# Performance work log

Hardware: AMD Instinct MI355X
Metric: run time of the kernel (lower is better)

Reference implementation:

```python
import jax, jax.numpy as jnp
import numpy as np

NEG = -1e4      # BigBird additive mask value
LN_EPS = 1e-12  # BERT-style LayerNorm eps


def _bigbird_forward(xs_pad, mask, Wq, bq, Wk, bk, Wv, bv, Wo, bo, gamma, beta, rand_idx):
    b, n, hsz = xs_pad.shape
    H = rand_idx.shape[0]
    nb = rand_idx.shape[1] + 2          # one rand row per non-edge query block
    BS = n // nb                        # block size
    d = hsz // H
    r = rand_idx.shape[2]
    scale = 1.0 / np.sqrt(d).astype(np.float32)

    mf = mask.reshape(b, n).astype(xs_pad.dtype)   # (b,n) 1=token, 0=pad
    mb = mf.reshape(b, nb, BS)                     # blocked mask

    def proj(W, bias):
        return (xs_pad @ W + bias).reshape(b, n, H, d).transpose(0, 2, 1, 3)

    q = proj(Wq, bq) * scale            # (b,H,n,d)
    k = proj(Wk, bk)
    v = proj(Wv, bv)
    qb = q.reshape(b, H, nb, BS, d)
    kb = k.reshape(b, H, nb, BS, d)
    vb = v.reshape(b, H, nb, BS, d)

    # ---- global rows: first / last query block attend to all keys ----
    def full_row(qi):                   # qi: (b,H,BS,d)
        s = jnp.einsum('bhqd,bhkd->bhqk', qi, k) + (1.0 - mf)[:, None, None, :] * NEG
        return jnp.einsum('bhqk,bhkd->bhqd', jax.nn.softmax(s, axis=-1), v)

    ctx_first = full_row(qb[:, :, 0])
    ctx_last = full_row(qb[:, :, nb - 1])

    # ---- random key/value blocks: per-head, per-query-block gather ----
    hidx = jnp.arange(H)[:, None, None]
    rand_k = kb[:, hidx, rand_idx].reshape(b, H, nb - 2, r * BS, d)
    rand_v = vb[:, hidx, rand_idx].reshape(b, H, nb - 2, r * BS, d)
    rand_m = mb[:, rand_idx].reshape(b, H, nb - 2, r * BS)

    def sparse_row(qi, kc, vc, mc):     # kc:(b,H,K,d), mc:(b,H,K)
        s = jnp.einsum('bhqd,bhkd->bhqk', qi, kc) + (1.0 - mc)[:, :, None, :] * NEG
        return jnp.einsum('bhqk,bhkd->bhqd', jax.nn.softmax(s, axis=-1), vc)

    def gather_blocks(ids, ridx):
        kc = jnp.concatenate([kb[:, :, j] for j in ids] + [rand_k[:, :, ridx]], axis=2)
        vc = jnp.concatenate([vb[:, :, j] for j in ids] + [rand_v[:, :, ridx]], axis=2)
        mc = jnp.concatenate([jnp.broadcast_to(mb[:, None, j], (b, H, BS)) for j in ids]
                             + [rand_m[:, :, ridx]], axis=2)
        return kc, vc, mc

    # second / penultimate query blocks: window + globals + rand
    ctx_second = sparse_row(qb[:, :, 1], *gather_blocks([0, 1, 2, nb - 1], 0))
    ctx_penult = sparse_row(qb[:, :, nb - 2], *gather_blocks([nb - 3, nb - 2, nb - 1, 0], nb - 3))

    # ---- middle rows i in [2, nb-3]: 3-block sliding window + first/last global + r random ----
    nmid = nb - 4
    mid = jnp.arange(2, nb - 2)
    win = mid[:, None] + jnp.arange(-1, 2)[None, :]        # (nmid,3)
    k_win = kb[:, :, win].reshape(b, H, nmid, 3 * BS, d)
    v_win = vb[:, :, win].reshape(b, H, nmid, 3 * BS, d)
    m_win = jnp.broadcast_to(mb[:, win].reshape(b, 1, nmid, 3 * BS), (b, H, nmid, 3 * BS))

    def rep_glob(t):                     # (b,H,BS,...) -> (b,H,nmid,BS,...)
        return jnp.broadcast_to(t[:, :, None], (b, H, nmid) + t.shape[2:])

    k_mid = jnp.concatenate([k_win, rep_glob(kb[:, :, 0]), rep_glob(kb[:, :, nb - 1]),
                             rand_k[:, :, 1:nb - 3]], axis=3)
    v_mid = jnp.concatenate([v_win, rep_glob(vb[:, :, 0]), rep_glob(vb[:, :, nb - 1]),
                             rand_v[:, :, 1:nb - 3]], axis=3)
    m_first = jnp.broadcast_to(mb[:, None, None, 0], (b, H, nmid, BS))
    m_last = jnp.broadcast_to(mb[:, None, None, nb - 1], (b, H, nmid, BS))
    m_mid = jnp.concatenate([m_win, m_first, m_last, rand_m[:, :, 1:nb - 3]], axis=3)

    s_mid = jnp.einsum('bhmqd,bhmkd->bhmqk', qb[:, :, 2:nb - 2], k_mid) \
            + (1.0 - m_mid)[:, :, :, None, :] * NEG
    ctx_mid = jnp.einsum('bhmqk,bhmkd->bhmqd', jax.nn.softmax(s_mid, axis=-1), v_mid)

    ctx = jnp.concatenate([ctx_first[:, :, None], ctx_second[:, :, None], ctx_mid,
                           ctx_penult[:, :, None], ctx_last[:, :, None]], axis=2)
    ctx = ctx.reshape(b, H, n, d).transpose(0, 2, 1, 3).reshape(b, n, hsz)
    ctx = ctx * mf[:, :, None]           # from_mask on output rows

    # BigBirdSelfOutput: dense + residual + LayerNorm (dropout=0 / eval)
    y = ctx @ Wo + bo + xs_pad
    mu = y.mean(-1, keepdims=True)
    var = ((y - mu) ** 2).mean(-1, keepdims=True)
    return (y - mu) * jax.lax.rsqrt(var + LN_EPS) * gamma + beta


def setup_inputs() -> dict:
    key = jax.random.key(0)
    ks = jax.random.split(key, 6)
    B, N, HSZ, H, BS, R = 4, 4096, 1024, 16, 64, 3
    NB = N // BS
    init = lambda k, shp: jax.random.normal(k, shp, dtype=jnp.float32) * 0.02
    return {
        'xs_pad': jax.random.normal(ks[0], (B, N, HSZ), dtype=jnp.float32),
        'mask': jnp.ones((B, 1, N), dtype=jnp.int32),
        'Wq': init(ks[1], (HSZ, HSZ)), 'bq': jnp.zeros((HSZ,), jnp.float32),
        'Wk': init(ks[2], (HSZ, HSZ)), 'bk': jnp.zeros((HSZ,), jnp.float32),
        'Wv': init(ks[3], (HSZ, HSZ)), 'bv': jnp.zeros((HSZ,), jnp.float32),
        'Wo': init(ks[4], (HSZ, HSZ)), 'bo': jnp.zeros((HSZ,), jnp.float32),
        'gamma': jnp.ones((HSZ,), jnp.float32), 'beta': jnp.zeros((HSZ,), jnp.float32),
        'rand_idx': jax.random.randint(ks[5], (H, NB - 2, R), 1, NB - 1).astype(jnp.int32),
    }


def reference(xs_pad, mask, Wq, bq, Wk, bk, Wv, bv, Wo, bo, gamma, beta, rand_idx):
    return _bigbird_forward(xs_pad, mask, Wq, bq, Wk, bk, Wv, bv, Wo, bo, gamma, beta, rand_idx)
```

## Files before the change

### kernel.cpp

```cpp
#include <hip/hip_runtime.h>
#include <hip/hip_bf16.h>

#define B_   4
#define N_   4096
#define HSZ  1024
#define H_   16
#define D_   64
#define NB_  64
#define R_   3
#define M_   (B_*N_)
#define NEGV (-1e4f)
#define LOG2E 1.4426950408889634f

typedef float f32x4 __attribute__((ext_vector_type(4)));
typedef short s16x8 __attribute__((ext_vector_type(8)));
typedef __bf16 b16x8 __attribute__((ext_vector_type(8)));

__device__ __forceinline__ f32x4 mfma16(s16x8 a, s16x8 b, f32x4 c) {
  return __builtin_amdgcn_mfma_f32_16x16x32_bf16(
      __builtin_bit_cast(b16x8, a), __builtin_bit_cast(b16x8, b), c, 0, 0, 0);
}

__device__ __forceinline__ short f2b(float x) {
  __hip_bfloat16 h = __float2bfloat16(x);
  return (short)__builtin_bit_cast(unsigned short, h);
}

__device__ __forceinline__ unsigned pack2(float a, float b) {
  return (unsigned)(unsigned short)f2b(a) |
         ((unsigned)(unsigned short)f2b(b) << 16);
}

__device__ __forceinline__ void gl_lds16(const short* g, short* l) {
  __builtin_amdgcn_global_load_lds(
      (const __attribute__((address_space(1))) unsigned int*)g,
      (__attribute__((address_space(3))) unsigned int*)l, 16, 0, 0);
}

__global__ __launch_bounds__(256) void k_prep(const float* __restrict__ in,
                                              short* __restrict__ out,
                                              const float* __restrict__ Wq,
                                              const float* __restrict__ Wk,
                                              const float* __restrict__ Wv,
                                              const float* __restrict__ Wo,
                                              short* __restrict__ wt) {
  const int tid = threadIdx.x;
  if (blockIdx.x < 8192) {
    size_t i = ((size_t)blockIdx.x * 256 + tid) * 8;
    float4 a = *(const float4*)&in[i];
    float4 b = *(const float4*)&in[i + 4];
    s16x8 o;
    o[0] = f2b(a.x); o[1] = f2b(a.y); o[2] = f2b(a.z); o[3] = f2b(a.w);
    o[4] = f2b(b.x); o[5] = f2b(b.y); o[6] = f2b(b.z); o[7] = f2b(b.w);
    *(s16x8*)&out[i] = o;
    return;
  }
  const int bid = blockIdx.x - 8192;
  const int z = bid >> 8;
  const int rest = bid & 255;
  const int tk = (rest >> 4) * 64, tn = (rest & 15) * 64;
  const float* src = (z == 0) ? Wq : (z == 1) ? Wk : (z == 2) ? Wv : Wo;
  short* dst = wt + (size_t)z * HSZ * HSZ;
  __shared__ __align__(16) float t[64][68];
#pragma unroll
  for (int r = 0; r < 4; ++r) {
    int c = tid + r * 256;
    int row = c >> 4, seg = c & 15;
    *(float4*)&t[row][seg * 4] =
        *(const float4*)&src[(size_t)(tk + row) * HSZ + tn + seg * 4];
  }
  __syncthreads();
#pragma unroll
  for (int r = 0; r < 2; ++r) {
    int c = tid + r * 256;
    int row = c >> 3, seg = c & 7;
    s16x8 o;
#pragma unroll
    for (int u = 0; u < 8; ++u) o[u] = f2b(t[seg * 8 + u][row]);
    *(s16x8*)&dst[(size_t)(tn + row) * HSZ + tk + seg * 8] = o;
  }
}

template <bool SWAP>
__device__ __forceinline__ void gemm8_core(
    const short* __restrict__ A, const short* __restrict__ Bt, int tm, int tn,
    short (&a_lds)[2][256][64], short (&b_lds)[2][256][64],
    f32x4 (&acc)[8][4], int wave, int lane) {
  const int lq = lane & 15, g = lane >> 4;
  const int wm = wave >> 2, wn = wave & 3;
  const int sl8 = lane >> 3;
  const int sc = ((lane & 7) ^ sl8) * 8;

  auto ST_A = [&](int buf, int kt) {
#pragma unroll
    for (int h = 0; h < 2; ++h)
#pragma unroll
      for (int u = 0; u < 2; ++u) {
        const int rbase = h * 128 + wave * 8 + u * 64;
        gl_lds16(&A[(size_t)(tm + rbase + sl8) * HSZ + kt * 64 + sc],
                 &a_lds[buf][rbase][0]);
      }
  };
  auto ST_B = [&](int buf, int kt) {
#pragma unroll
    for (int h = 0; h < 2; ++h)
#pragma unroll
      for (int u = 0; u < 2; ++u) {
        const int rbase = h * 128 + wave * 8 + u * 64;
        gl_lds16(&Bt[(size_t)(tn + rbase + sl8) * HSZ + kt * 64 + sc],
                 &b_lds[buf][rbase][0]);
      }
  };

  s16x8 bf[4][2];
  auto LOADB = [&](int buf) {
#pragma unroll
    for (int j = 0; j < 4; ++j) {
      const int row = wn * 64 + j * 16 + lq;
#pragma unroll
      for (int kk = 0; kk < 2; ++kk)
        bf[j][kk] =
            *(const s16x8*)&b_lds[buf][row][((kk * 4 + g) ^ (lq & 7)) * 8];
    }
  };
  s16x8 afc[2][2], afn[2][2];
  auto LOADA = [&](int buf, int m0, s16x8 (&af)[2][2]) {
#pragma unroll
    for (int i = 0; i < 2; ++i) {
      const int row = wm * 128 + (m0 + i) * 16 + lq;
#pragma unroll
      for (int kk = 0; kk < 2; ++kk)
        af[i][kk] =
            *(const s16x8*)&a_lds[buf][row][((kk * 4 + g) ^ (lq & 7)) * 8];
    }
  };
  auto MF = [&](s16x8 (&af)[2][2], int m0) {
    __builtin_amdgcn_s_setprio(1);
#pragma unroll
    for (int i = 0; i < 2; ++i)
#pragma unroll
      for (int j = 0; j < 4; ++j)
#pragma unroll
        for (int kk = 0; kk < 2; ++kk)
          acc[m0 + i][j] = SWAP
                               ? mfma16(bf[j][kk], af[i][kk], acc[m0 + i][j])
                               : mfma16(af[i][kk], bf[j][kk], acc[m0 + i][j]);
    __builtin_amdgcn_s_setprio(0);
    __builtin_amdgcn_s_barrier();
  };

  ST_A(0, 0);
  ST_B(0, 0);
  ST_B(1, 1);

  for (int p = 0; p < 8; ++p) {
    const int t = 2 * p;
    ST_A(1, t + 1);
    asm volatile("s_waitcnt vmcnt(8)" ::: "memory");
    __builtin_amdgcn_s_barrier();
    LOADB(0);
    LOADA(0, 0, afc);
    LOADA(0, 2, afn);
    MF(afc, 0);
    if (t + 2 < 16) ST_B(0, t + 2);
    LOADA(0, 4, afc);
    MF(afn, 2);
    LOADA(0, 6, afn);
    MF(afc, 4);
    MF(afn, 6);
    if (t + 2 < 16) ST_A(0, t + 2);
    if (p < 7) {
      asm volatile("s_waitcnt vmcnt(8)" ::: "memory");
    } else {
      asm volatile("s_waitcnt vmcnt(0)" ::: "memory");
    }
    __builtin_amdgcn_s_barrier();
    LOADB(1);
    LOADA(1, 0, afc);
    LOADA(1, 2, afn);
    MF(afc, 0);
    if (t + 3 < 16) ST_B(1, t + 3);
    LOADA(1, 4, afc);
    MF(afn, 2);
    LOADA(1, 6, afn);
    MF(afc, 4);
    MF(afn, 6);
  }
}

__global__ __launch_bounds__(512) void k_qkv(
    const short* __restrict__ A, const short* __restrict__ WT,
    const float* __restrict__ bq, const float* __restrict__ bk,
    const float* __restrict__ bv, short* __restrict__ oq,
    short* __restrict__ ok, short* __restrict__ ovt) {
  const int orig = blockIdx.x;
  const int xcd = orig & 7, r = orig >> 3;
  const int combo = r >> 3, tml = r & 7;
  const int z = combo >> 2, tnl = combo & 3;
  const int tm = (xcd * 8 + tml) * 256, tn = tnl * 256;
  const short* Bt = WT + (size_t)z * HSZ * HSZ;

  __shared__ __align__(16) short a_lds[2][256][64];
  __shared__ __align__(16) short b_lds[2][256][64];

  const int tid = threadIdx.x, lane = tid & 63, wave = tid >> 6;
  const int lq = lane & 15, g = lane >> 4;
  const int wm = wave >> 2, wn = wave & 3;

  f32x4 acc[8][4] = {};

  if (z == 2) {
    gemm8_core<false>(A, Bt, tm, tn, a_lds, b_lds, acc, wave, lane);
#pragma unroll
    for (int j = 0; j < 4; ++j) {
      const int col = tn + wn * 64 + j * 16 + lq;
      const int hh = col >> 6, dd = col & 63;
      const float bi = bv[col];
#pragma unroll
      for (int i = 0; i < 8; ++i) {
        const int nrow = tm + wm * 128 + i * 16 + g * 4;
        const int bb = nrow >> 12, nn = nrow & (N_ - 1);
        uint2 w;
        w.x = pack2(acc[i][j][0] + bi, acc[i][j][1] + bi);
        w.y = pack2(acc[i][j][2] + bi, acc[i][j][3] + bi);
        *(uint2*)&ovt[(((size_t)bb * H_ + hh) * D_ + dd) * N_ + nn] = w;
      }
    }
  } else {
    gemm8_core<true>(A, Bt, tm, tn, a_lds, b_lds, acc, wave, lane);
    const float* bias = z ? bk : bq;
    short* outb = z ? ok : oq;
    const float alpha = z ? 1.0f : 0.125f * LOG2E;
#pragma unroll
    for (int i = 0; i < 8; ++i) {
      const int row = tm + wm * 128 + i * 16 + lq;
#pragma unroll
      for (int j = 0; j < 4; ++j) {
        const int colb = tn + wn * 64 + j * 16 + g * 4;
        const float4 bi = *(const float4*)&bias[colb];
        const int bb = row >> 12, nn = row & (N_ - 1);
        const int hh = colb >> 6, dd = colb & 63;
        uint2 w;
        w.x = pack2((acc[i][j][0] + bi.x) * alpha,
                    (acc[i][j][1] + bi.y) * alpha);
        w.y = pack2((acc[i][j][2] + bi.z) * alpha,
                    (acc[i][j][3] + bi.w) * alpha);
        *(uint2*)&outb[(((size_t)bb * H_ + hh) * N_ + nn) * D_ + dd] = w;
      }
    }
  }
}

__global__ __launch_bounds__(512) void k_out(
    const short* __restrict__ A, const short* __restrict__ WT,
    const float* __restrict__ bo, const float* __restrict__ xs,
    float* __restrict__ yout) {
  const short* Bt = WT + (size_t)3 * HSZ * HSZ;

  __shared__ __align__(16) short a_lds[2][256][64];
  __shared__ __align__(16) short b_lds[2][256][64];

  const int tid = threadIdx.x, lane = tid & 63, wave = tid >> 6;
  const int lq = lane & 15, g = lane >> 4;
  const int wm = wave >> 2, wn = wave & 3;
  const int orig = blockIdx.x;
  const int xcd = orig & 7, r = orig >> 3;
  const int tnl = r >> 3, tml = r & 7;
  const int tm = (xcd * 8 + tml) * 256, tn = tnl * 256;

  f32x4 acc[8][4] = {};
  gemm8_core<true>(A, Bt, tm, tn, a_lds, b_lds, acc, wave, lane);

#pragma unroll
  for (int i = 0; i < 8; ++i) {
    const int row = tm + wm * 128 + i * 16 + lq;
#pragma unroll
    for (int j = 0; j < 4; ++j) {
      const int colb = tn + wn * 64 + j * 16 + g * 4;
      const float4 bi = *(const float4*)&bo[colb];
      const size_t idx = (size_t)row * HSZ + colb;
      const float4 xv = *(const float4*)&xs[idx];
      float4 yv;
      yv.x = acc[i][j][0] + bi.x + xv.x;
      yv.y = acc[i][j][1] + bi.y + xv.y;
      yv.z = acc[i][j][2] + bi.z + xv.z;
      yv.w = acc[i][j][3] + bi.w + xv.w;
      *(float4*)&yout[idx] = yv;
    }
  }
}

__global__ __launch_bounds__(256) void k_attn(
    const short* __restrict__ Q, const short* __restrict__ K,
    const short* __restrict__ VT, const int* __restrict__ mask,
    const int* __restrict__ rnd, short* __restrict__ ctx,
    float* __restrict__ pO, float* __restrict__ pm, float* __restrict__ pl) {
  const int orig = blockIdx.x;
  const int swg = (orig & 7) * 624 + (orig >> 3);
  const int s = swg % 78;
  const int bh_i = swg / 78;
  const int h = bh_i & 15, b = bh_i >> 4;
  const int tid = threadIdx.x, lane = tid & 63, wave = tid >> 6;
  const int g = lane >> 4, lq = lane & 15;

  __shared__ __align__(16) short k_lds[2][64][64];
  __shared__ __align__(16) short vt_lds[2][64][64];
  __shared__ __align__(16) short p_lds[4][16][72];
  __shared__ __align__(16) float bias_s[8][64];
  __shared__ int list_s[8];
  __shared__ int Ls;

  const bool mid = (s < 62);
  const int qb = mid ? (s + 1) : (((s - 62) >> 3) ? (NB_ - 1) : 0);

  if (tid == 0) {
    int L;
    if (!mid) {
      int chunk = (s - 62) & 7;
#pragma unroll
      for (int i = 0; i < 8; ++i) list_s[i] = chunk * 8 + i;
      L = 8;
    } else {
      const int* rp = rnd + ((size_t)h * (NB_ - 2) + (qb - 1)) * R_;
      int n;
      if (qb == 1) {
        list_s[0] = 0; list_s[1] = 1; list_s[2] = 2; list_s[3] = NB_ - 1; n = 4;
      } else if (qb == NB_ - 2) {
        list_s[0] = NB_ - 3; list_s[1] = NB_ - 2; list_s[2] = NB_ - 1;
        list_s[3] = 0; n = 4;
      } else {
        list_s[0] = qb - 1; list_s[1] = qb; list_s[2] = qb + 1;
        list_s[3] = 0; list_s[4] = NB_ - 1; n = 5;
      }
      for (int j = 0; j < R_; ++j) list_s[n + j] = rp[j];
      L = n + R_;
      for (int i = L; i < 8; ++i) list_s[i] = 0;
    }
    Ls = L;
  }

  const size_t bh = (size_t)b * H_ + h;
  const size_t qrow = bh * N_ + (size_t)qb * 64 + wave * 16 + lq;
  s16x8 qf0 = *(const s16x8*)&Q[qrow * D_ + g * 8];
  s16x8 qf1 = *(const s16x8*)&Q[qrow * D_ + 32 + g * 8];

  __syncthreads();
  const int L = Ls;

  const int sw = (lq & 7);
  const int sl8 = lane >> 3;
  const int scg = ((lane & 7) ^ sl8) * 8;

  const short* Kb = K + bh * (size_t)N_ * D_;
  const short* Vb = VT + bh * (size_t)D_ * N_;
  const int* mb = mask + (size_t)b * N_;

  for (int t = tid; t < 512; t += 256) {
    const int i = t >> 6, kk2 = t & 63;
    bias_s[i][kk2] =
        (1.0f - (float)mb[list_s[i] * 64 + kk2]) * (NEGV * LOG2E);
  }
  asm volatile("s_waitcnt lgkmcnt(0)" ::: "memory");

  auto STAGE = [&](int buf, int kb) {
    const short* kp = Kb + (size_t)kb * 64 * D_;
    const short* vp = Vb + (size_t)kb * 64;
#pragma unroll
    for (int u = 0; u < 2; ++u) {
      const int rb = wave * 16 + u * 8;
      gl_lds16(&kp[(size_t)(rb + sl8) * D_ + scg], &k_lds[buf][rb][0]);
      gl_lds16(&vp[(size_t)(rb + sl8) * N_ + scg], &vt_lds[buf][rb][0]);
    }
  };

  s16x8 ones;
#pragma unroll
  for (int u = 0; u < 8; ++u) ones[u] = (short)0x3F80;

  f32x4 o[4] = {};
  f32x4 osum = {};
  float mshift = 0.0f;

  STAGE(0, list_s[0]);

  for (int it = 0; it < L; ++it) {
    const int buf = it & 1;
    if (it + 1 < L) {
      STAGE(buf ^ 1, list_s[it + 1]);
      asm volatile("s_waitcnt vmcnt(4)" ::: "memory");
    } else {
      asm volatile("s_waitcnt vmcnt(0)" ::: "memory");
    }
    __builtin_amdgcn_s_barrier();

    f32x4 st[4];
#pragma unroll
    for (int f = 0; f < 4; ++f) {
      f32x4 a0 = *(const f32x4*)&bias_s[it][f * 16 + g * 4];
      s16x8 af0 = *(const s16x8*)&k_lds[buf][f * 16 + lq][(g ^ sw) * 8];
      s16x8 af1 = *(const s16x8*)&k_lds[buf][f * 16 + lq][((4 + g) ^ sw) * 8];
      a0 = mfma16(af0, qf0, a0);
      a0 = mfma16(af1, qf1, a0);
      st[f] = a0;
    }

    if (mshift == 0.0f) {
#pragma unroll
      for (int f = 0; f < 4; ++f)
#pragma unroll
        for (int e = 0; e < 4; ++e) st[f][e] = exp2f(st[f][e]);
    } else {
#pragma unroll
      for (int f = 0; f < 4; ++f)
#pragma unroll
        for (int e = 0; e < 4; ++e) st[f][e] = exp2f(st[f][e] - mshift);
    }

#pragma unroll
    for (int f = 0; f < 4; ++f) {
      uint2 w = make_uint2(pack2(st[f][0], st[f][1]),
                           pack2(st[f][2], st[f][3]));
      *(uint2*)&p_lds[wave][lq][f * 16 + g * 4] = w;
    }

#pragma unroll
    for (int kk = 0; kk < 2; ++kk) {
      s16x8 pa = *(const s16x8*)&p_lds[wave][lq][kk * 32 + g * 8];
#pragma unroll
      for (int j = 0; j < 4; ++j) {
        s16x8 bv =
            *(const s16x8*)&vt_lds[buf][j * 16 + lq][((kk * 4 + g) ^ sw) * 8];
        o[j] = mfma16(pa, bv, o[j]);
      }
      osum = mfma16(pa, ones, osum);
    }

    float om = fmaxf(fmaxf(osum[0], osum[1]), fmaxf(osum[2], osum[3]));
    if (__any(om > 16777216.0f)) {
#pragma unroll
      for (int j = 0; j < 4; ++j) o[j] *= 5.9604645e-08f;
      osum *= 5.9604645e-08f;
      mshift += 24.0f;
    }
    __builtin_amdgcn_s_barrier();
  }

  if (mid) {
    float rs[4];
#pragma unroll
    for (int e = 0; e < 4; ++e)
      rs[e] = (float)mb[qb * 64 + wave * 16 + g * 4 + e] /
              fmaxf(osum[e], 1e-30f);
    __syncthreads();
    short (*ost)[64] = k_lds[0];
#pragma unroll
    for (int j = 0; j < 4; ++j) {
      ost[wave * 16 + g * 4 + 0][j * 16 + lq] = f2b(o[j][0] * rs[0]);
      ost[wave * 16 + g * 4 + 1][j * 16 + lq] = f2b(o[j][1] * rs[1]);
      ost[wave * 16 + g * 4 + 2][j * 16 + lq] = f2b(o[j][2] * rs[2]);
      ost[wave * 16 + g * 4 + 3][j * 16 + lq] = f2b(o[j][3] * rs[3]);
    }
    __syncthreads();
#pragma unroll
    for (int pp = 0; pp < 2; ++pp) {
      int c = tid + pp * 256;
      int row = c >> 3, seg = c & 7;
      *(s16x8*)&ctx[((size_t)b * N_ + qb * 64 + row) * HSZ + h * D_ + seg * 8] =
          *(const s16x8*)&ost[row][seg * 8];
    }
  } else {
    const int e2 = s - 62;
    const int qsel = e2 >> 3, chunk = e2 & 7;
    const size_t eidx = (bh * 2 + qsel) * 8 + chunk;
    float* po = pO + eidx * 4096;
#pragma unroll
    for (int j = 0; j < 4; ++j)
#pragma unroll
      for (int e = 0; e < 4; ++e)
        po[(wave * 16 + g * 4 + e) * 64 + j * 16 + lq] = o[j][e];
    if (lq == 0) {
#pragma unroll
      for (int e = 0; e < 4; ++e) {
        pm[eidx * 64 + wave * 16 + g * 4 + e] = mshift;
        pl[eidx * 64 + wave * 16 + g * 4 + e] = osum[e];
      }
    }
  }
}

__global__ __launch_bounds__(256) void k_comb(
    const float* __restrict__ pO, const float* __restrict__ pm,
    const float* __restrict__ pl, const int* __restrict__ mask,
    short* __restrict__ ctx) {
  const int qsel = blockIdx.x, h = blockIdx.y, b = blockIdx.z;
  const int qb = qsel ? NB_ - 1 : 0;
  const int tid = threadIdx.x;
  const int q = tid >> 2, dq = tid & 3;
  const size_t base = (((size_t)b * H_ + h) * 2 + qsel) * 8;

  float mv[8];
  float M = -INFINITY;
#pragma unroll
  for (int i = 0; i < 8; ++i) {
    mv[i] = pm[(base + i) * 64 + q];
    M = fmaxf(M, mv[i]);
  }
  float Lsum = 0.0f;
#pragma unroll
  for (int i = 0; i < 8; ++i) {
    float w = exp2f(mv[i] - M);
    mv[i] = w;
    Lsum += pl[(base + i) * 64 + q] * w;
  }
  f32x4 acc[4] = {};
#pragma unroll
  for (int i = 0; i < 8; ++i) {
    const float* p = pO + (base + i) * 4096 + q * 64 + dq * 16;
    float w = mv[i];
#pragma unroll
    for (int u = 0; u < 4; ++u) {
      f32x4 v = *(const f32x4*)&p[u * 4];
      acc[u] += v * w;
    }
  }
  float sc = (float)mask[(size_t)b * N_ + qb * 64 + q] / fmaxf(Lsum, 1e-30f);
  s16x8 out0, out1;
#pragma unroll
  for (int u = 0; u < 8; ++u) {
    out0[u] = f2b(acc[u >> 2][u & 3] * sc);
    out1[u] = f2b(acc[2 + (u >> 2)][u & 3] * sc);
  }
  short* dst = &ctx[((size_t)b * N_ + qb * 64 + q) * HSZ + h * D_ + dq * 16];
  *(s16x8*)dst = out0;
  *(s16x8*)(dst + 8) = out1;
}

__global__ __launch_bounds__(256) void k_ln(float* __restrict__ y,
                                            const float* __restrict__ gamma,
                                            const float* __restrict__ beta) {
  const int row = blockIdx.x, tid = threadIdx.x, lane = tid & 63,
            wave = tid >> 6;
  __shared__ float s_sum[4], s_sq[4];
  float4 v = *(const float4*)&y[(size_t)row * HSZ + tid * 4];
  float s = v.x + v.y + v.z + v.w;
  float q = v.x * v.x + v.y * v.y + v.z * v.z + v.w * v.w;
#pragma unroll
  for (int m = 1; m <= 32; m <<= 1) {
    s += __shfl_xor(s, m);
    q += __shfl_xor(q, m);
  }
  if (lane == 0) { s_sum[wave] = s; s_sq[wave] = q; }
  __syncthreads();
  float S = s_sum[0] + s_sum[1] + s_sum[2] + s_sum[3];
  float Qs = s_sq[0] + s_sq[1] + s_sq[2] + s_sq[3];
  float mu = S * (1.0f / HSZ);
  float var = Qs * (1.0f / HSZ) - mu * mu;
  float r = rsqrtf(var + 1e-12f);
  float4 g = *(const float4*)&gamma[tid * 4];
  float4 be = *(const float4*)&beta[tid * 4];
  float4 outv;
  outv.x = (v.x - mu) * r * g.x + be.x;
  outv.y = (v.y - mu) * r * g.y + be.y;
  outv.z = (v.z - mu) * r * g.z + be.z;
  outv.w = (v.w - mu) * r * g.w + be.w;
  *(float4*)&y[(size_t)row * HSZ + tid * 4] = outv;
}

extern "C" void kernel_launch(void* const* d_in, const int* in_sizes, int n_in,
                              void* d_out, int out_size, void* d_ws,
                              size_t ws_size, hipStream_t stream) {
  const float* xs = (const float*)d_in[0];
  const int* mask = (const int*)d_in[1];
  const float* Wq = (const float*)d_in[2];
  const float* bq = (const float*)d_in[3];
  const float* Wk = (const float*)d_in[4];
  const float* bk = (const float*)d_in[5];
  const float* Wv = (const float*)d_in[6];
  const float* bv = (const float*)d_in[7];
  const float* Wo = (const float*)d_in[8];
  const float* bo = (const float*)d_in[9];
  const float* gamma = (const float*)d_in[10];
  const float* beta = (const float*)d_in[11];
  const int* rnd = (const int*)d_in[12];
  float* yout = (float*)d_out;

  char* ws = (char*)d_ws;
  const size_t SZ_XS = (size_t)M_ * HSZ * 2;
  const size_t SZ_WT = (size_t)4 * HSZ * HSZ * 2;
  short* xsb = (short*)ws;
  short* wt = (short*)(ws + SZ_XS);
  short* qbuf = (short*)(ws + SZ_XS + SZ_WT);
  short* kbuf = qbuf + (size_t)M_ * HSZ;
  short* vtb = kbuf + (size_t)M_ * HSZ;
  char* after = ws + SZ_XS + SZ_WT + 3 * SZ_XS;
  float* pO = (float*)(after + (1 << 20));
  float* pm = pO + (size_t)1024 * 4096;
  float* pl = pm + (size_t)1024 * 64;

  k_prep<<<9216, 256, 0, stream>>>(xs, xsb, Wq, Wk, Wv, Wo, wt);
  k_qkv<<<768, 512, 0, stream>>>(xsb, wt, bq, bk, bv, qbuf, kbuf, vtb);
  k_attn<<<4992, 256, 0, stream>>>(qbuf, kbuf, vtb, mask, rnd, xsb, pO, pm,
                                   pl);
  k_comb<<<dim3(2, H_, B_), 256, 0, stream>>>(pO, pm, pl, mask, xsb);
  k_out<<<256, 512, 0, stream>>>(xsb, wt, bo, xs, yout);
  k_ln<<<M_, 256, 0, stream>>>(yout, gamma, beta);
}
```

Baseline: 320.3 us.

## Replace double-buffered GEMM LDS pipeline with single-buffer load-then-compute loop

```diff
diff --git a/kernel.cpp b/kernel.cpp
--- a/kernel.cpp
+++ b/kernel.cpp
@@ -82,56 +82,56 @@
 }
 
 template <bool SWAP>
-__device__ __forceinline__ void gemm8_core(
+__device__ __forceinline__ void gemm_sb_core(
     const short* __restrict__ A, const short* __restrict__ Bt, int tm, int tn,
-    short (&a_lds)[2][256][64], short (&b_lds)[2][256][64],
+    short (&a_lds)[256][64], short (&b_lds)[256][64],
     f32x4 (&acc)[8][4], int wave, int lane) {
   const int lq = lane & 15, g = lane >> 4;
   const int wm = wave >> 2, wn = wave & 3;
   const int sl8 = lane >> 3;
   const int sc = ((lane & 7) ^ sl8) * 8;
 
-  auto ST_A = [&](int buf, int kt) {
+  auto ST_A = [&](int kt) {
 #pragma unroll
     for (int h = 0; h < 2; ++h)
 #pragma unroll
       for (int u = 0; u < 2; ++u) {
         const int rbase = h * 128 + wave * 8 + u * 64;
         gl_lds16(&A[(size_t)(tm + rbase + sl8) * HSZ + kt * 64 + sc],
-                 &a_lds[buf][rbase][0]);
+                 &a_lds[rbase][0]);
       }
   };
-  auto ST_B = [&](int buf, int kt) {
+  auto ST_B = [&](int kt) {
 #pragma unroll
     for (int h = 0; h < 2; ++h)
 #pragma unroll
       for (int u = 0; u < 2; ++u) {
         const int rbase = h * 128 + wave * 8 + u * 64;
         gl_lds16(&Bt[(size_t)(tn + rbase + sl8) * HSZ + kt * 64 + sc],
-                 &b_lds[buf][rbase][0]);
+                 &b_lds[rbase][0]);
       }
   };
 
   s16x8 bf[4][2];
-  auto LOADB = [&](int buf) {
+  auto LOADB = [&]() {
 #pragma unroll
     for (int j = 0; j < 4; ++j) {
       const int row = wn * 64 + j * 16 + lq;
 #pragma unroll
       for (int kk = 0; kk < 2; ++kk)
         bf[j][kk] =
-            *(const s16x8*)&b_lds[buf][row][((kk * 4 + g) ^ (lq & 7)) * 8];
+            *(const s16x8*)&b_lds[row][((kk * 4 + g) ^ (lq & 7)) * 8];
     }
   };
   s16x8 afc[2][2], afn[2][2];
-  auto LOADA = [&](int buf, int m0, s16x8 (&af)[2][2]) {
+  auto LOADA = [&](int m0, s16x8 (&af)[2][2]) {
 #pragma unroll
     for (int i = 0; i < 2; ++i) {
       const int row = wm * 128 + (m0 + i) * 16 + lq;
 #pragma unroll
       for (int kk = 0; kk < 2; ++kk)
         af[i][kk] =
-            *(const s16x8*)&a_lds[buf][row][((kk * 4 + g) ^ (lq & 7)) * 8];
+            *(const s16x8*)&a_lds[row][((kk * 4 + g) ^ (lq & 7)) * 8];
     }
   };
   auto MF = [&](s16x8 (&af)[2][2], int m0) {
@@ -146,45 +146,28 @@
                                ? mfma16(bf[j][kk], af[i][kk], acc[m0 + i][j])
                                : mfma16(af[i][kk], bf[j][kk], acc[m0 + i][j]);
     __builtin_amdgcn_s_setprio(0);
+  };
+
+  ST_A(0);
+  ST_B(0);
+
+  for (int t = 0; t < 16; ++t) {
+    asm volatile("s_waitcnt vmcnt(0)" ::: "memory");
     __builtin_amdgcn_s_barrier();
-  };
-
-  ST_A(0, 0);
-  ST_B(0, 0);
-  ST_B(1, 1);
-
-  for (int p = 0; p < 8; ++p) {
-    const int t = 2 * p;
-    ST_A(1, t + 1);
-    asm volatile("s_waitcnt vmcnt(8)" ::: "memory");
-    __builtin_amdgcn_s_barrier();
-    LOADB(0);
-    LOADA(0, 0, afc);
-    LOADA(0, 2, afn);
+    LOADB();
+    LOADA(0, afc);
+    LOADA(2, afn);
     MF(afc, 0);
-    if (t + 2 < 16) ST_B(0, t + 2);
-    LOADA(0, 4, afc);
+    LOADA(4, afc);
     MF(afn, 2);
-    LOADA(0, 6, afn);
+    LOADA(6, afn);
     MF(afc, 4);
     MF(afn, 6);
-    if (t + 2 < 16) ST_A(0, t + 2);
-    if (p < 7) {
-      asm volatile("s_waitcnt vmcnt(8)" ::: "memory");
-    } else {
-      asm volatile("s_waitcnt vmcnt(0)" ::: "memory");
-    }
     __builtin_amdgcn_s_barrier();
-    LOADB(1);
-    LOADA(1, 0, afc);
-    LOADA(1, 2, afn);
-    MF(afc, 0);
-    if (t + 3 < 16) ST_B(1, t + 3);
-    LOADA(1, 4, afc);
-    MF(afn, 2);
-    LOADA(1, 6, afn);
-    MF(afc, 4);
-    MF(afn, 6);
+    if (t < 15) {
+      ST_A(t + 1);
+      ST_B(t + 1);
+    }
   }
 }
 
@@ -200,8 +183,8 @@
   const int tm = (xcd * 8 + tml) * 256, tn = tnl * 256;
   const short* Bt = WT + (size_t)z * HSZ * HSZ;
 
-  __shared__ __align__(16) short a_lds[2][256][64];
-  __shared__ __align__(16) short b_lds[2][256][64];
+  __shared__ __align__(16) short a_lds[256][64];
+  __shared__ __align__(16) short b_lds[256][64];
 
   const int tid = threadIdx.x, lane = tid & 63, wave = tid >> 6;
   const int lq = lane & 15, g = lane >> 4;
@@ -210,7 +193,7 @@
   f32x4 acc[8][4] = {};
 
   if (z == 2) {
-    gemm8_core<false>(A, Bt, tm, tn, a_lds, b_lds, acc, wave, lane);
+    gemm_sb_core<false>(A, Bt, tm, tn, a_lds, b_lds, acc, wave, lane);
 #pragma unroll
     for (int j = 0; j < 4; ++j) {
       const int col = tn + wn * 64 + j * 16 + lq;
@@ -227,7 +210,7 @@
       }
     }
   } else {
-    gemm8_core<true>(A, Bt, tm, tn, a_lds, b_lds, acc, wave, lane);
+    gemm_sb_core<true>(A, Bt, tm, tn, a_lds, b_lds, acc, wave, lane);
     const float* bias = z ? bk : bq;
     short* outb = z ? ok : oq;
     const float alpha = z ? 1.0f : 0.125f * LOG2E;
@@ -257,8 +240,8 @@
     float* __restrict__ yout) {
   const short* Bt = WT + (size_t)3 * HSZ * HSZ;
 
-  __shared__ __align__(16) short a_lds[2][256][64];
-  __shared__ __align__(16) short b_lds[2][256][64];
+  __shared__ __align__(16) short a_lds[256][64];
+  __shared__ __align__(16) short b_lds[256][64];
 
   const int tid = threadIdx.x, lane = tid & 63, wave = tid >> 6;
   const int lq = lane & 15, g = lane >> 4;
@@ -269,7 +252,7 @@
   const int tm = (xcd * 8 + tml) * 256, tn = tnl * 256;
 
   f32x4 acc[8][4] = {};
-  gemm8_core<true>(A, Bt, tm, tn, a_lds, b_lds, acc, wave, lane);
+  gemm_sb_core<true>(A, Bt, tm, tn, a_lds, b_lds, acc, wave, lane);
 
 #pragma unroll
   for (int i = 0; i < 8; ++i) {
```

After: 336.5 us. +5.1%, slower.
